# Kernel tuning notes

Measured on AMD Instinct MI355X. Metric: run time of the kernel, lower is better.

## Reference

```python
import jax, jax.numpy as jnp
import numpy as np

B = 8192
E = 8
H = 128
NUM_CLASSES = 3
SIM_THRESHOLD = 0.8
EFF_THRESHOLD = 0.1
TARGET_TEMP = 1.0
W_LB, W_EFF, W_CONS, W_ENT, W_TEMP = 0.1, 0.05, 0.1, 0.01, 0.01


def setup_inputs() -> dict:
    key = jax.random.key(0)
    k1, k2, k3, k4 = jax.random.split(key, 4)
    logits = jax.random.normal(k1, (B, NUM_CLASSES), dtype=jnp.float32)
    targets = jax.random.randint(k2, (B,), 0, NUM_CLASSES, dtype=jnp.int64)
    raw = jax.random.uniform(k3, (B, E), dtype=jnp.float32)
    routing_probs = raw / raw.sum(axis=-1, keepdims=True)  # rows sum to 1
    input_embeddings = jax.random.uniform(k4, (B, H), dtype=jnp.float32)
    temperature = jnp.ones((1,), dtype=jnp.float32)
    return {
        "logits": logits,
        "targets": targets,
        "routing_probs": routing_probs,
        "input_embeddings": input_embeddings,
        "temperature": temperature,
    }


def _dynamo_loss(logits, routing_probs, input_embeddings, temperature, targets):
    # --- task loss: cross entropy (sentiment) ---
    logp_cls = jax.nn.log_softmax(logits, axis=-1)
    task_loss = -jnp.take_along_axis(logp_cls, targets[:, None], axis=-1).mean()

    # --- load balance: var(mean usage) / (1/E)^2 (torch.var unbiased) ---
    expert_usage = routing_probs.mean(axis=0)  # [E]
    lb_loss = W_LB * jnp.var(expert_usage, ddof=1) * (E ** 2)

    # --- efficiency: sum of probs below threshold, averaged over batch ---
    small = jnp.where(routing_probs < EFF_THRESHOLD, routing_probs, 0.0)
    eff_loss = W_EFF * small.sum(axis=-1).mean()

    # --- consistency: masked pairwise KL over similar samples ---
    nrm = input_embeddings / jnp.linalg.norm(input_embeddings, axis=-1, keepdims=True)
    sim = nrm @ nrm.T  # [B, B]
    mask = (sim > SIM_THRESHOLD) & ~jnp.eye(B, dtype=bool)
    logp = jax.nn.log_softmax(routing_probs, axis=-1)  # [B, E]
    p = jnp.exp(logp)
    a = jnp.sum(p * logp, axis=-1)  # [B], sum_e p_j log p_j
    # KL(i,j) = sum_e p_j (log p_j - log p_i) = a[j] - logp[i] . p[j]
    kl = a[None, :] - logp @ p.T  # [B, B]
    num_pairs = mask.sum()
    kl_sum = jnp.sum(jnp.where(mask, kl, 0.0))
    cons_loss = W_CONS * jnp.where(num_pairs > 0, kl_sum / jnp.maximum(num_pairs, 1), 0.0)

    # --- entropy regularization (maximize entropy of routing_probs-as-probs) ---
    eps = 1e-8
    entropy = -jnp.sum(routing_probs * jnp.log(routing_probs + eps), axis=-1)
    ent_loss = W_ENT * (-entropy.mean())

    # --- temperature regularization ---
    temp_loss = W_TEMP * jnp.mean((temperature - TARGET_TEMP) ** 2)

    return task_loss + lb_loss + eff_loss + cons_loss + ent_loss + temp_loss


def reference(logits, targets, routing_probs, input_embeddings, temperature):
    return _dynamo_loss(logits, routing_probs, input_embeddings, temperature, targets)
```

## Files before the change

### kernel.cpp

```cpp
#include <hip/hip_runtime.h>
#include <stdint.h>

#define B_SZ 8192
#define LOG8 2.0794415416798357f
#define NCHUNK 544

typedef __attribute__((ext_vector_type(8))) short short8;
typedef __attribute__((ext_vector_type(4))) float floatx4;

typedef __attribute__((address_space(1))) const uint4 guint4;
typedef __attribute__((address_space(3))) uint4 luint4;

__device__ inline void async_cp16(const uint4* g, uint4* l) {
    __builtin_amdgcn_global_load_lds((guint4*)g, (luint4*)l, 16, 0, 0);
}

__device__ inline unsigned short f2bf(float f) {
    unsigned int u = __float_as_uint(f);
    u = (u + 0x7FFFu + ((u >> 16) & 1u)) >> 16;
    return (unsigned short)u;
}
__device__ inline float bf2f(unsigned short s) {
    return __uint_as_float(((unsigned int)s) << 16);
}
__device__ inline float wredf(float x) {
#pragma unroll
    for (int o = 32; o; o >>= 1) x += __shfl_down(x, o);
    return x;
}
__device__ inline int wredi(int x) {
#pragma unroll
    for (int o = 32; o; o >>= 1) x += __shfl_down(x, o);
    return x;
}


__global__ __launch_bounds__(512) void prep_all(
    const float* __restrict__ logits,
    const int* __restrict__ targets,
    const float* __restrict__ routing,
    const float* __restrict__ emb,
    unsigned short* __restrict__ nrm,
    unsigned short* __restrict__ nlq,
    unsigned short* __restrict__ pb,
    float* __restrict__ aprime,
    float* __restrict__ prepslot) {
    __shared__ float pred[8][11];
    const int bid = blockIdx.x;
    const int lane = threadIdx.x & 63;
    const int wave = threadIdx.x >> 6;

    if (bid < 256) {
#pragma unroll
        for (int iter = 0; iter < 4; ++iter) {
            int row = (((iter << 8) + bid) << 3) + wave;
            const float2* e2 = (const float2*)(emb + (size_t)row * 128);
            float2 v = e2[lane];
            float ss = v.x * v.x + v.y * v.y;
            ss = wredf(ss);
            ss = __shfl(ss, 0);
            float inv = rsqrtf(ss);
            ushort2 o;
            o.x = f2bf(v.x * inv);
            o.y = f2bf(v.y * inv);
            ((ushort2*)(nrm + (size_t)row * 128))[lane] = o;
        }
        return;
    }

    int row = ((bid - 256) << 9) + threadIdx.x;

    const float4* r4 = (const float4*)(routing + (size_t)row * 8);
    float4 va = r4[0], vb = r4[1];
    float v[8] = {va.x, va.y, va.z, va.w, vb.x, vb.y, vb.z, vb.w};

    float mx = v[0];
#pragma unroll
    for (int e = 1; e < 8; ++e) mx = fmaxf(mx, v[e]);
    float ex[8], s = 0.f;
#pragma unroll
    for (int e = 0; e < 8; ++e) { ex[e] = expf(v[e] - mx); s += ex[e]; }
    float ls = logf(s);
    float inv_s = 1.f / s;

    union { unsigned short u[8]; uint4 q; } lu, pu;
    float ap = 0.f;
#pragma unroll
    for (int e = 0; e < 8; ++e) {
        unsigned short pe = f2bf(ex[e] * inv_s);
        unsigned short le = f2bf(v[e] - mx - ls + LOG8);
        pu.u[e] = pe;
        lu.u[e] = le ^ 0x8000;
        ap += bf2f(pe) * bf2f(le);
    }
    ((uint4*)nlq)[row] = lu.q;
    ((uint4*)pb)[row] = pu.q;
    aprime[row] = ap;

    float eff = 0.f, ent = 0.f;
#pragma unroll
    for (int e = 0; e < 8; ++e) {
        if (v[e] < 0.1f) eff += v[e];
        ent += v[e] * logf(v[e] + 1e-8f);
    }

    const float* lg = logits + (size_t)row * 3;
    float a0 = lg[0], a1 = lg[1], a2 = lg[2];
    float mm = fmaxf(a0, fmaxf(a1, a2));
    float lse = mm + logf(expf(a0 - mm) + expf(a1 - mm) + expf(a2 - mm));
    int tg = targets[row];
    float tv = (tg == 0) ? a0 : ((tg == 1) ? a1 : a2);
    float task = lse - tv;

    task = wredf(task);
    eff = wredf(eff);
    ent = wredf(ent);
    float cs[8];
#pragma unroll
    for (int e = 0; e < 8; ++e) cs[e] = wredf(v[e]);

    if (lane == 0) {
        pred[wave][0] = task;
        pred[wave][1] = eff;
        pred[wave][2] = ent;
#pragma unroll
        for (int e = 0; e < 8; ++e) pred[wave][3 + e] = cs[e];
    }
    __syncthreads();
    if (threadIdx.x < 11) {
        float s2 = 0.f;
#pragma unroll
        for (int w = 0; w < 8; ++w) s2 += pred[w][threadIdx.x];
        prepslot[(bid - 256) * 11 + threadIdx.x] = s2;
    }
}

__global__ __launch_bounds__(512, 4) void tile_sym(
    const unsigned short* __restrict__ nrm,
    const unsigned short* __restrict__ nlq,
    const unsigned short* __restrict__ pb,
    const float* __restrict__ aprime,
    float* __restrict__ klslot,
    unsigned int* __restrict__ cntslot) {
    __shared__ uint4 sh[4096];

    const int t = threadIdx.x;
    const int wave = t >> 6, lane = t & 63;

    int bi = 0, rem = blockIdx.x;
    for (;;) {
        int nc = (135 - 2 * bi) >> 3;
        if (rem < nc) break;
        rem -= nc;
        ++bi;
    }
    const int c = rem;
    const int bj0 = 2 * bi + (c << 3);
    const int nt = min(8, 128 - bj0);
    const int iBase = bi << 7;

    const uint4* n4 = (const uint4*)nrm;

#pragma unroll
    for (int it = 0; it < 4; ++it) {
        int idx = t + (it << 9);
        int row = idx >> 4, s = idx & 15;
        int g = s ^ (row & 15);
        async_cp16(&n4[((size_t)(iBase + row) << 4) + g],
                   sh + (it << 9) + (wave << 6));
    }
    {
        const int jB = bj0 << 6;
#pragma unroll
        for (int it = 0; it < 2; ++it) {
            int idx = t + (it << 9);
            int row = idx >> 4, s = idx & 15;
            int g = s ^ (row & 15);
            async_cp16(&n4[((size_t)(jB + row) << 4) + g],
                       sh + 2048 + (it << 9) + (wave << 6));
        }
    }

    const int wr = wave >> 2, wc = wave & 3;
    const int m = lane & 15, q = lane >> 4;
    const short8 zero8 = (short8){0, 0, 0, 0, 0, 0, 0, 0};

    short8 crA[4];
#pragma unroll
    for (int a = 0; a < 4; ++a) {
        int ri = iBase + (wr << 6) + (a << 4) + m;
        short8 v = zero8;
        if (q == 0) v = *(const short8*)&nlq[(size_t)ri << 3];
        else if (q == 1) v = *(const short8*)&pb[(size_t)ri << 3];
        else if (q == 2) {
            v[0] = (short)f2bf(aprime[ri]);
            v[1] = (short)0x3F80;
        }
        crA[a] = v;
    }

    __syncthreads();

    float klLocal = 0.f;
    int cntLocal = 0;

#pragma unroll 1
    for (int tt = 0; tt < nt; ++tt) {
        const int bj = bj0 + tt;
        const int jBase = bj << 6;
        const bool strip = ((bj >> 1) == bi);
        const int cur = 2048 + ((tt & 1) << 10);

        if (tt + 1 < nt) {
            const int jN = (bj + 1) << 6;
            const int nxt = 2048 + (((tt + 1) & 1) << 10);
#pragma unroll
            for (int it = 0; it < 2; ++it) {
                int idx = t + (it << 9);
                int row = idx >> 4, s = idx & 15;
                int g = s ^ (row & 15);
                async_cp16(&n4[((size_t)(jN + row) << 4) + g],
                           sh + nxt + (it << 9) + (wave << 6));
            }
        }

        short8 crB;
        {
            int cj = jBase + (wc << 4) + m;
            short8 v = zero8;
            if (q == 0) v = *(const short8*)&pb[(size_t)cj << 3];
            else if (q == 1) v = *(const short8*)&nlq[(size_t)cj << 3];
            else if (q == 2) {
                v[0] = (short)0x3F80;
                v[1] = (short)f2bf(aprime[cj]);
            }
            crB = v;
        }

        floatx4 simacc[4];
#pragma unroll
        for (int a = 0; a < 4; ++a) simacc[a] = (floatx4){0.f, 0.f, 0.f, 0.f};
#pragma unroll
        for (int ks = 0; ks < 4; ++ks) {
            const int gk = (ks << 2) + q;
            short8 bfr;
            {
                int rb = (wc << 4) + m;
                bfr = *(const short8*)(sh + cur + (rb << 4) + (gk ^ m));
            }
            short8 af[4];
#pragma unroll
            for (int a = 0; a < 4; ++a) {
                int row = (wr << 6) + (a << 4) + m;
                af[a] = *(const short8*)(sh + (row << 4) + (gk ^ m));
            }
#pragma unroll
            for (int a = 0; a < 4; ++a)
                simacc[a] = __builtin_amdgcn_mfma_f32_16x16x32_bf16(
                    af[a], bfr, simacc[a], 0, 0, 0);
        }

        const int gCol = jBase + (wc << 4) + m;
#pragma unroll
        for (int a = 0; a < 4; ++a) {
            short8 ca = crA[a];
            if (strip) {
                if (q == 1) ca = zero8;
                else if (q == 2) ca[0] = 0;
            }
            floatx4 cr = __builtin_amdgcn_mfma_f32_16x16x32_bf16(
                ca, crB, (floatx4){0.f, 0.f, 0.f, 0.f}, 0, 0, 0);
            const int gRow0 = iBase + (wr << 6) + (a << 4) + (q << 2);
            if (strip) {
#pragma unroll
                for (int r = 0; r < 4; ++r) {
                    if ((simacc[a][r] > 0.8f) && (gRow0 + r != gCol)) {
                        klLocal += cr[r];
                        cntLocal += 1;
                    }
                }
            } else {
#pragma unroll
                for (int r = 0; r < 4; ++r) {
                    if (simacc[a][r] > 0.8f) {
                        klLocal += cr[r];
                        cntLocal += 2;
                    }
                }
            }
        }

        __syncthreads();
    }

    klLocal = wredf(klLocal);
    cntLocal = wredi(cntLocal);

    float* redk = (float*)sh;
    int* redc = (int*)(redk + 8);
    if (lane == 0) { redk[wave] = klLocal; redc[wave] = cntLocal; }
    __syncthreads();

    if (t == 0) {
        float k = 0.f;
        int cc = 0;
#pragma unroll
        for (int w = 0; w < 8; ++w) { k += redk[w]; cc += redc[w]; }
        klslot[blockIdx.x] = k;
        cntslot[blockIdx.x] = (unsigned int)cc;
    }
}

__global__ void finalize_k(const float* __restrict__ klslot,
                           const unsigned int* __restrict__ cntslot,
                           const float* __restrict__ prepslot,
                           const float* __restrict__ temp,
                           float* __restrict__ out) {
    __shared__ float sk[4];
    __shared__ int sc[4];
    __shared__ float sp[11];
    const int t = threadIdx.x, lane = t & 63, wave = t >> 6;

    float k = 0.f;
    int c = 0;
    for (int i = t; i < NCHUNK; i += 256) { k += klslot[i]; c += (int)cntslot[i]; }
    k = wredf(k);
    c = wredi(c);
    if (lane == 0) { sk[wave] = k; sc[wave] = c; }
    if (t < 11) {
        float s = 0.f;
        for (int r = 0; r < 16; ++r) s += prepslot[r * 11 + t];
        sp[t] = s;
    }
    __syncthreads();
    if (t == 0) {
        float K = sk[0] + sk[1] + sk[2] + sk[3];
        int C = sc[0] + sc[1] + sc[2] + sc[3];
        const float invB = 1.f / (float)B_SZ;
        float task = sp[0] * invB;
        float eff = 0.05f * sp[1] * invB;
        float entl = 0.01f * sp[2] * invB;
        float cons = 0.1f * (C > 0 ? K / (float)C : 0.f);
        float u[8], mean = 0.f;
        for (int e = 0; e < 8; ++e) { u[e] = sp[3 + e] * invB; mean += u[e]; }
        mean *= 0.125f;
        float var = 0.f;
        for (int e = 0; e < 8; ++e) { float d = u[e] - mean; var += d * d; }
        var *= (1.f / 7.f);
        float lb = 0.1f * var * 64.f;
        float tt = temp[0] - 1.f;
        out[0] = task + lb + eff + cons + entl + 0.01f * tt * tt;
    }
}

extern "C" void kernel_launch(void* const* d_in, const int* in_sizes, int n_in,
                              void* d_out, int out_size, void* d_ws, size_t ws_size,
                              hipStream_t stream) {
    const float* logits = (const float*)d_in[0];
    const int* targets = (const int*)d_in[1];
    const float* routing = (const float*)d_in[2];
    const float* emb = (const float*)d_in[3];
    const float* temp = (const float*)d_in[4];

    char* ws = (char*)d_ws;
    unsigned short* nrm = (unsigned short*)ws;
    unsigned short* nlq = (unsigned short*)(ws + 2097152);
    unsigned short* pb = (unsigned short*)(ws + 2228224);
    float* aprime = (float*)(ws + 2359296);
    float* klslot = (float*)(ws + 2392064);
    unsigned int* cntslot = (unsigned int*)(ws + 2394304);
    float* prepslot = (float*)(ws + 2396544);

    prep_all<<<272, 512, 0, stream>>>(logits, targets, routing, emb,
                                      nrm, nlq, pb, aprime, prepslot);
    tile_sym<<<NCHUNK, 512, 0, stream>>>(nrm, nlq, pb, aprime, klslot, cntslot);
    finalize_k<<<1, 256, 0, stream>>>(klslot, cntslot, prepslot, temp,
                                      (float*)d_out);
}
```

Baseline: 105.9 us.

## Fuse prep, tile and finalize into one persistent kernel with grid barrier

Merges the three launches into a single persistent kernel of 512 blocks. Each block first normalizes its slice of rows, then all blocks meet at an atomic-counter grid barrier, pull tile chunks from an atomic work queue, and the last block to finish does the final reduction. This removes two kernel launch gaps and the separate finalize pass. In exchange it relies on all 512 blocks being co-resident for the spin barrier, and it adds a memset plus atomic contention.

```diff
diff --git a/kernel.cpp b/kernel.cpp
--- a/kernel.cpp
+++ b/kernel.cpp
@@ -3,7 +3,8 @@
 
 #define B_SZ 8192
 #define LOG8 2.0794415416798357f
-#define NCHUNK 544
+#define NCHUNKS 544
+#define NBLK 512
 
 typedef __attribute__((ext_vector_type(8))) short short8;
 typedef __attribute__((ext_vector_type(4))) float floatx4;
@@ -35,321 +36,335 @@
 }
 
 
-__global__ __launch_bounds__(512) void prep_all(
+__global__ __launch_bounds__(512, 4) void fused_all(
     const float* __restrict__ logits,
     const int* __restrict__ targets,
     const float* __restrict__ routing,
     const float* __restrict__ emb,
+    const float* __restrict__ temp,
     unsigned short* __restrict__ nrm,
     unsigned short* __restrict__ nlq,
     unsigned short* __restrict__ pb,
     float* __restrict__ aprime,
-    float* __restrict__ prepslot) {
-    __shared__ float pred[8][11];
+    float* __restrict__ klslot,
+    unsigned int* __restrict__ cntslot,
+    float* __restrict__ prepcol,
+    unsigned int* __restrict__ ctrl,
+    float* __restrict__ out) {
+    __shared__ uint4 sh[4096];
+    __shared__ int msgSh;
+
+    const int t = threadIdx.x;
+    const int lane = t & 63, wave = t >> 6;
     const int bid = blockIdx.x;
-    const int lane = threadIdx.x & 63;
-    const int wave = threadIdx.x >> 6;
-
-    if (bid < 256) {
-#pragma unroll
-        for (int iter = 0; iter < 4; ++iter) {
-            int row = (((iter << 8) + bid) << 3) + wave;
-            const float2* e2 = (const float2*)(emb + (size_t)row * 128);
-            float2 v = e2[lane];
-            float ss = v.x * v.x + v.y * v.y;
-            ss = wredf(ss);
-            ss = __shfl(ss, 0);
-            float inv = rsqrtf(ss);
-            ushort2 o;
-            o.x = f2bf(v.x * inv);
-            o.y = f2bf(v.y * inv);
-            ((ushort2*)(nrm + (size_t)row * 128))[lane] = o;
-        }
-        return;
-    }
-
-    int row = ((bid - 256) << 9) + threadIdx.x;
-
-    const float4* r4 = (const float4*)(routing + (size_t)row * 8);
-    float4 va = r4[0], vb = r4[1];
-    float v[8] = {va.x, va.y, va.z, va.w, vb.x, vb.y, vb.z, vb.w};
-
-    float mx = v[0];
-#pragma unroll
-    for (int e = 1; e < 8; ++e) mx = fmaxf(mx, v[e]);
-    float ex[8], s = 0.f;
-#pragma unroll
-    for (int e = 0; e < 8; ++e) { ex[e] = expf(v[e] - mx); s += ex[e]; }
-    float ls = logf(s);
-    float inv_s = 1.f / s;
-
-    union { unsigned short u[8]; uint4 q; } lu, pu;
-    float ap = 0.f;
-#pragma unroll
-    for (int e = 0; e < 8; ++e) {
-        unsigned short pe = f2bf(ex[e] * inv_s);
-        unsigned short le = f2bf(v[e] - mx - ls + LOG8);
-        pu.u[e] = pe;
-        lu.u[e] = le ^ 0x8000;
-        ap += bf2f(pe) * bf2f(le);
-    }
-    ((uint4*)nlq)[row] = lu.q;
-    ((uint4*)pb)[row] = pu.q;
-    aprime[row] = ap;
-
-    float eff = 0.f, ent = 0.f;
-#pragma unroll
-    for (int e = 0; e < 8; ++e) {
-        if (v[e] < 0.1f) eff += v[e];
-        ent += v[e] * logf(v[e] + 1e-8f);
-    }
-
-    const float* lg = logits + (size_t)row * 3;
-    float a0 = lg[0], a1 = lg[1], a2 = lg[2];
-    float mm = fmaxf(a0, fmaxf(a1, a2));
-    float lse = mm + logf(expf(a0 - mm) + expf(a1 - mm) + expf(a2 - mm));
-    int tg = targets[row];
-    float tv = (tg == 0) ? a0 : ((tg == 1) ? a1 : a2);
-    float task = lse - tv;
-
-    task = wredf(task);
-    eff = wredf(eff);
-    ent = wredf(ent);
-    float cs[8];
-#pragma unroll
-    for (int e = 0; e < 8; ++e) cs[e] = wredf(v[e]);
-
-    if (lane == 0) {
-        pred[wave][0] = task;
-        pred[wave][1] = eff;
-        pred[wave][2] = ent;
-#pragma unroll
-        for (int e = 0; e < 8; ++e) pred[wave][3 + e] = cs[e];
-    }
+
+#pragma unroll
+    for (int i = 0; i < 2; ++i) {
+        int row = (bid << 4) + (wave << 1) + i;
+        const float2* e2 = (const float2*)(emb + (size_t)row * 128);
+        float2 v = e2[lane];
+        float ss = v.x * v.x + v.y * v.y;
+        ss = wredf(ss);
+        ss = __shfl(ss, 0);
+        float inv = rsqrtf(ss);
+        ushort2 o;
+        o.x = f2bf(v.x * inv);
+        o.y = f2bf(v.y * inv);
+        ((ushort2*)(nrm + (size_t)row * 128))[lane] = o;
+    }
+
+    float acc11[11];
+#pragma unroll
+    for (int k = 0; k < 11; ++k) acc11[k] = 0.f;
+    if (t < 16) {
+        int row = (bid << 4) + t;
+        const float4* r4 = (const float4*)(routing + (size_t)row * 8);
+        float4 va = r4[0], vb = r4[1];
+        float v[8] = {va.x, va.y, va.z, va.w, vb.x, vb.y, vb.z, vb.w};
+
+        float mx = v[0];
+#pragma unroll
+        for (int e = 1; e < 8; ++e) mx = fmaxf(mx, v[e]);
+        float ex[8], s = 0.f;
+#pragma unroll
+        for (int e = 0; e < 8; ++e) { ex[e] = expf(v[e] - mx); s += ex[e]; }
+        float ls = logf(s);
+        float inv_s = 1.f / s;
+
+        union { unsigned short u[8]; uint4 q; } lu, pu;
+        float ap = 0.f;
+#pragma unroll
+        for (int e = 0; e < 8; ++e) {
+            unsigned short pe = f2bf(ex[e] * inv_s);
+            unsigned short le = f2bf(v[e] - mx - ls + LOG8);
+            pu.u[e] = pe;
+            lu.u[e] = le ^ 0x8000;
+            ap += bf2f(pe) * bf2f(le);
+        }
+        ((uint4*)nlq)[row] = lu.q;
+        ((uint4*)pb)[row] = pu.q;
+        aprime[row] = ap;
+
+        float eff = 0.f, ent = 0.f;
+#pragma unroll
+        for (int e = 0; e < 8; ++e) {
+            if (v[e] < 0.1f) eff += v[e];
+            ent += v[e] * logf(v[e] + 1e-8f);
+            acc11[3 + e] = v[e];
+        }
+
+        const float* lg = logits + (size_t)row * 3;
+        float a0 = lg[0], a1 = lg[1], a2 = lg[2];
+        float mm = fmaxf(a0, fmaxf(a1, a2));
+        float lse = mm + logf(expf(a0 - mm) + expf(a1 - mm) + expf(a2 - mm));
+        int tg = targets[row];
+        float tv = (tg == 0) ? a0 : ((tg == 1) ? a1 : a2);
+        acc11[0] = lse - tv;
+        acc11[1] = eff;
+        acc11[2] = ent;
+    }
+    if (wave == 0) {
+#pragma unroll
+        for (int k = 0; k < 11; ++k) acc11[k] = wredf(acc11[k]);
+        if (lane == 0) {
+#pragma unroll
+            for (int k = 0; k < 11; ++k) prepcol[k * NBLK + bid] = acc11[k];
+        }
+    }
+
     __syncthreads();
-    if (threadIdx.x < 11) {
-        float s2 = 0.f;
-#pragma unroll
-        for (int w = 0; w < 8; ++w) s2 += pred[w][threadIdx.x];
-        prepslot[(bid - 256) * 11 + threadIdx.x] = s2;
-    }
-}
-
-__global__ __launch_bounds__(512, 4) void tile_sym(
-    const unsigned short* __restrict__ nrm,
-    const unsigned short* __restrict__ nlq,
-    const unsigned short* __restrict__ pb,
-    const float* __restrict__ aprime,
-    float* __restrict__ klslot,
-    unsigned int* __restrict__ cntslot) {
-    __shared__ uint4 sh[4096];
-
-    const int t = threadIdx.x;
-    const int wave = t >> 6, lane = t & 63;
-
-    int bi = 0, rem = blockIdx.x;
+    if (t == 0) {
+        __threadfence();
+        atomicAdd(&ctrl[0], 1u);
+        while (__hip_atomic_load(&ctrl[0], __ATOMIC_ACQUIRE,
+                                 __HIP_MEMORY_SCOPE_AGENT) < NBLK) {}
+    }
+    __syncthreads();
+
+    const uint4* n4 = (const uint4*)nrm;
+    const int wr = wave >> 2, wc = wave & 3;
+    const int m = lane & 15, q = lane >> 4;
+    const short8 zero8 = (short8){0, 0, 0, 0, 0, 0, 0, 0};
+
+    float klLocal = 0.f;
+    int cntLocal = 0;
+
+#pragma unroll 1
     for (;;) {
-        int nc = (135 - 2 * bi) >> 3;
-        if (rem < nc) break;
-        rem -= nc;
-        ++bi;
-    }
-    const int c = rem;
-    const int bj0 = 2 * bi + (c << 3);
-    const int nt = min(8, 128 - bj0);
-    const int iBase = bi << 7;
-
-    const uint4* n4 = (const uint4*)nrm;
-
-#pragma unroll
-    for (int it = 0; it < 4; ++it) {
-        int idx = t + (it << 9);
-        int row = idx >> 4, s = idx & 15;
-        int g = s ^ (row & 15);
-        async_cp16(&n4[((size_t)(iBase + row) << 4) + g],
-                   sh + (it << 9) + (wave << 6));
-    }
-    {
-        const int jB = bj0 << 6;
-#pragma unroll
-        for (int it = 0; it < 2; ++it) {
+        if (t == 0) msgSh = (int)atomicAdd(&ctrl[1], 1u);
+        __syncthreads();
+        const int chunk = msgSh;
+        if (chunk >= NCHUNKS) break;
+
+        int bi = 0, rem = chunk;
+        for (;;) {
+            int nc = (135 - 2 * bi) >> 3;
+            if (rem < nc) break;
+            rem -= nc;
+            ++bi;
+        }
+        const int bj0 = 2 * bi + (rem << 3);
+        const int nt = min(8, 128 - bj0);
+        const int iBase = bi << 7;
+
+#pragma unroll
+        for (int it = 0; it < 4; ++it) {
             int idx = t + (it << 9);
             int row = idx >> 4, s = idx & 15;
             int g = s ^ (row & 15);
-            async_cp16(&n4[((size_t)(jB + row) << 4) + g],
-                       sh + 2048 + (it << 9) + (wave << 6));
-        }
-    }
-
-    const int wr = wave >> 2, wc = wave & 3;
-    const int m = lane & 15, q = lane >> 4;
-    const short8 zero8 = (short8){0, 0, 0, 0, 0, 0, 0, 0};
-
-    short8 crA[4];
-#pragma unroll
-    for (int a = 0; a < 4; ++a) {
-        int ri = iBase + (wr << 6) + (a << 4) + m;
-        short8 v = zero8;
-        if (q == 0) v = *(const short8*)&nlq[(size_t)ri << 3];
-        else if (q == 1) v = *(const short8*)&pb[(size_t)ri << 3];
-        else if (q == 2) {
-            v[0] = (short)f2bf(aprime[ri]);
-            v[1] = (short)0x3F80;
-        }
-        crA[a] = v;
-    }
-
-    __syncthreads();
-
-    float klLocal = 0.f;
-    int cntLocal = 0;
-
-#pragma unroll 1
-    for (int tt = 0; tt < nt; ++tt) {
-        const int bj = bj0 + tt;
-        const int jBase = bj << 6;
-        const bool strip = ((bj >> 1) == bi);
-        const int cur = 2048 + ((tt & 1) << 10);
-
-        if (tt + 1 < nt) {
-            const int jN = (bj + 1) << 6;
-            const int nxt = 2048 + (((tt + 1) & 1) << 10);
+            async_cp16(&n4[((size_t)(iBase + row) << 4) + g],
+                       sh + (it << 9) + (wave << 6));
+        }
+        {
+            const int jB = bj0 << 6;
 #pragma unroll
             for (int it = 0; it < 2; ++it) {
                 int idx = t + (it << 9);
                 int row = idx >> 4, s = idx & 15;
                 int g = s ^ (row & 15);
-                async_cp16(&n4[((size_t)(jN + row) << 4) + g],
-                           sh + nxt + (it << 9) + (wave << 6));
-            }
-        }
-
-        short8 crB;
-        {
-            int cj = jBase + (wc << 4) + m;
+                async_cp16(&n4[((size_t)(jB + row) << 4) + g],
+                           sh + 2048 + (it << 9) + (wave << 6));
+            }
+        }
+
+        short8 crA[4];
+#pragma unroll
+        for (int a = 0; a < 4; ++a) {
+            int ri = iBase + (wr << 6) + (a << 4) + m;
             short8 v = zero8;
-            if (q == 0) v = *(const short8*)&pb[(size_t)cj << 3];
-            else if (q == 1) v = *(const short8*)&nlq[(size_t)cj << 3];
+            if (q == 0) v = *(const short8*)&nlq[(size_t)ri << 3];
+            else if (q == 1) v = *(const short8*)&pb[(size_t)ri << 3];
             else if (q == 2) {
-                v[0] = (short)0x3F80;
-                v[1] = (short)f2bf(aprime[cj]);
-            }
-            crB = v;
-        }
-
-        floatx4 simacc[4];
-#pragma unroll
-        for (int a = 0; a < 4; ++a) simacc[a] = (floatx4){0.f, 0.f, 0.f, 0.f};
-#pragma unroll
-        for (int ks = 0; ks < 4; ++ks) {
-            const int gk = (ks << 2) + q;
-            short8 bfr;
+                v[0] = (short)f2bf(aprime[ri]);
+                v[1] = (short)0x3F80;
+            }
+            crA[a] = v;
+        }
+
+        __syncthreads();
+
+#pragma unroll 1
+        for (int tt = 0; tt < nt; ++tt) {
+            const int bj = bj0 + tt;
+            const int jBase = bj << 6;
+            const bool strip = ((bj >> 1) == bi);
+            const int cur = 2048 + ((tt & 1) << 10);
+
+            if (tt + 1 < nt) {
+                const int jN = (bj + 1) << 6;
+                const int nxt = 2048 + (((tt + 1) & 1) << 10);
+#pragma unroll
+                for (int it = 0; it < 2; ++it) {
+                    int idx = t + (it << 9);
+                    int row = idx >> 4, s = idx & 15;
+                    int g = s ^ (row & 15);
+                    async_cp16(&n4[((size_t)(jN + row) << 4) + g],
+                               sh + nxt + (it << 9) + (wave << 6));
+                }
+            }
+
+            short8 crB;
             {
-                int rb = (wc << 4) + m;
-                bfr = *(const short8*)(sh + cur + (rb << 4) + (gk ^ m));
-            }
-            short8 af[4];
+                int cj = jBase + (wc << 4) + m;
+                short8 v = zero8;
+                if (q == 0) v = *(const short8*)&pb[(size_t)cj << 3];
+                else if (q == 1) v = *(const short8*)&nlq[(size_t)cj << 3];
+                else if (q == 2) {
+                    v[0] = (short)0x3F80;
+                    v[1] = (short)f2bf(aprime[cj]);
+                }
+                crB = v;
+            }
+
+            floatx4 simacc[4];
+#pragma unroll
+            for (int a = 0; a < 4; ++a) simacc[a] = (floatx4){0.f, 0.f, 0.f, 0.f};
+#pragma unroll
+            for (int ks = 0; ks < 4; ++ks) {
+                const int gk = (ks << 2) + q;
+                short8 bfr;
+                {
+                    int rb = (wc << 4) + m;
+                    bfr = *(const short8*)(sh + cur + (rb << 4) + (gk ^ m));
+                }
+                short8 af[4];
+#pragma unroll
+                for (int a = 0; a < 4; ++a) {
+                    int row = (wr << 6) + (a << 4) + m;
+                    af[a] = *(const short8*)(sh + (row << 4) + (gk ^ m));
+                }
+#pragma unroll
+                for (int a = 0; a < 4; ++a)
+                    simacc[a] = __builtin_amdgcn_mfma_f32_16x16x32_bf16(
+                        af[a], bfr, simacc[a], 0, 0, 0);
+            }
+
+            const int gCol = jBase + (wc << 4) + m;
 #pragma unroll
             for (int a = 0; a < 4; ++a) {
-                int row = (wr << 6) + (a << 4) + m;
-                af[a] = *(const short8*)(sh + (row << 4) + (gk ^ m));
-            }
-#pragma unroll
-            for (int a = 0; a < 4; ++a)
-                simacc[a] = __builtin_amdgcn_mfma_f32_16x16x32_bf16(
-                    af[a], bfr, simacc[a], 0, 0, 0);
-        }
-
-        const int gCol = jBase + (wc << 4) + m;
-#pragma unroll
-        for (int a = 0; a < 4; ++a) {
-            short8 ca = crA[a];
-            if (strip) {
-                if (q == 1) ca = zero8;
-                else if (q == 2) ca[0] = 0;
-            }
-            floatx4 cr = __builtin_amdgcn_mfma_f32_16x16x32_bf16(
-                ca, crB, (floatx4){0.f, 0.f, 0.f, 0.f}, 0, 0, 0);
-            const int gRow0 = iBase + (wr << 6) + (a << 4) + (q << 2);
-            if (strip) {
-#pragma unroll
-                for (int r = 0; r < 4; ++r) {
-                    if ((simacc[a][r] > 0.8f) && (gRow0 + r != gCol)) {
-                        klLocal += cr[r];
-                        cntLocal += 1;
+                short8 ca = crA[a];
+                if (strip) {
+                    if (q == 1) ca = zero8;
+                    else if (q == 2) ca[0] = 0;
+                }
+                floatx4 cr = __builtin_amdgcn_mfma_f32_16x16x32_bf16(
+                    ca, crB, (floatx4){0.f, 0.f, 0.f, 0.f}, 0, 0, 0);
+                const int gRow0 = iBase + (wr << 6) + (a << 4) + (q << 2);
+                if (strip) {
+#pragma unroll
+                    for (int r = 0; r < 4; ++r) {
+                        if ((simacc[a][r] > 0.8f) && (gRow0 + r != gCol)) {
+                            klLocal += cr[r];
+                            cntLocal += 1;
+                        }
                     }
-                }
-            } else {
-#pragma unroll
-                for (int r = 0; r < 4; ++r) {
-                    if (simacc[a][r] > 0.8f) {
-                        klLocal += cr[r];
-                        cntLocal += 2;
+                } else {
+#pragma unroll
+                    for (int r = 0; r < 4; ++r) {
+                        if (simacc[a][r] > 0.8f) {
+                            klLocal += cr[r];
+                            cntLocal += 2;
+                        }
                     }
                 }
             }
-        }
-
-        __syncthreads();
+
+            __syncthreads();
+        }
     }
 
     klLocal = wredf(klLocal);
     cntLocal = wredi(cntLocal);
-
     float* redk = (float*)sh;
     int* redc = (int*)(redk + 8);
     if (lane == 0) { redk[wave] = klLocal; redc[wave] = cntLocal; }
     __syncthreads();
-
     if (t == 0) {
         float k = 0.f;
-        int cc = 0;
-#pragma unroll
-        for (int w = 0; w < 8; ++w) { k += redk[w]; cc += redc[w]; }
-        klslot[blockIdx.x] = k;
-        cntslot[blockIdx.x] = (unsigned int)cc;
-    }
-}
-
-__global__ void finalize_k(const float* __restrict__ klslot,
-                           const unsigned int* __restrict__ cntslot,
-                           const float* __restrict__ prepslot,
-                           const float* __restrict__ temp,
-                           float* __restrict__ out) {
-    __shared__ float sk[4];
-    __shared__ int sc[4];
-    __shared__ float sp[11];
-    const int t = threadIdx.x, lane = t & 63, wave = t >> 6;
-
-    float k = 0.f;
-    int c = 0;
-    for (int i = t; i < NCHUNK; i += 256) { k += klslot[i]; c += (int)cntslot[i]; }
-    k = wredf(k);
-    c = wredi(c);
-    if (lane == 0) { sk[wave] = k; sc[wave] = c; }
-    if (t < 11) {
-        float s = 0.f;
-        for (int r = 0; r < 16; ++r) s += prepslot[r * 11 + t];
-        sp[t] = s;
+        int c = 0;
+#pragma unroll
+        for (int w = 0; w < 8; ++w) { k += redk[w]; c += redc[w]; }
+        klslot[bid] = k;
+        cntslot[bid] = (unsigned int)c;
+        __threadfence();
+        unsigned int old = atomicAdd(&ctrl[2], 1u);
+        msgSh = (old == NBLK - 1);
     }
     __syncthreads();
-    if (t == 0) {
-        float K = sk[0] + sk[1] + sk[2] + sk[3];
-        int C = sc[0] + sc[1] + sc[2] + sc[3];
-        const float invB = 1.f / (float)B_SZ;
-        float task = sp[0] * invB;
-        float eff = 0.05f * sp[1] * invB;
-        float entl = 0.01f * sp[2] * invB;
-        float cons = 0.1f * (C > 0 ? K / (float)C : 0.f);
-        float u[8], mean = 0.f;
-        for (int e = 0; e < 8; ++e) { u[e] = sp[3 + e] * invB; mean += u[e]; }
-        mean *= 0.125f;
-        float var = 0.f;
-        for (int e = 0; e < 8; ++e) { float d = u[e] - mean; var += d * d; }
-        var *= (1.f / 7.f);
-        float lb = 0.1f * var * 64.f;
-        float tt = temp[0] - 1.f;
-        out[0] = task + lb + eff + cons + entl + 0.01f * tt * tt;
+
+    if (msgSh) {
+        float k = __hip_atomic_load(&klslot[t], __ATOMIC_RELAXED,
+                                    __HIP_MEMORY_SCOPE_AGENT);
+        int c = (int)__hip_atomic_load(&cntslot[t], __ATOMIC_RELAXED,
+                                       __HIP_MEMORY_SCOPE_AGENT);
+        float pv[11];
+#pragma unroll
+        for (int kk = 0; kk < 11; ++kk)
+            pv[kk] = __hip_atomic_load(&prepcol[kk * NBLK + t], __ATOMIC_RELAXED,
+                                       __HIP_MEMORY_SCOPE_AGENT);
+        k = wredf(k);
+        c = wredi(c);
+#pragma unroll
+        for (int kk = 0; kk < 11; ++kk) pv[kk] = wredf(pv[kk]);
+
+        float* rk = (float*)sh;
+        int* rc = (int*)(rk + 8);
+        float* rp = (float*)(rc + 8);
+        if (lane == 0) {
+            rk[wave] = k;
+            rc[wave] = c;
+#pragma unroll
+            for (int kk = 0; kk < 11; ++kk) rp[wave * 11 + kk] = pv[kk];
+        }
+        __syncthreads();
+        if (t == 0) {
+            float K = 0.f;
+            int C = 0;
+            float sp[11];
+#pragma unroll
+            for (int kk = 0; kk < 11; ++kk) sp[kk] = 0.f;
+#pragma unroll
+            for (int w = 0; w < 8; ++w) {
+                K += rk[w];
+                C += rc[w];
+#pragma unroll
+                for (int kk = 0; kk < 11; ++kk) sp[kk] += rp[w * 11 + kk];
+            }
+            const float invB = 1.f / (float)B_SZ;
+            float task = sp[0] * invB;
+            float eff = 0.05f * sp[1] * invB;
+            float entl = 0.01f * sp[2] * invB;
+            float cons = 0.1f * (C > 0 ? K / (float)C : 0.f);
+            float u[8], mean = 0.f;
+            for (int e = 0; e < 8; ++e) { u[e] = sp[3 + e] * invB; mean += u[e]; }
+            mean *= 0.125f;
+            float var = 0.f;
+            for (int e = 0; e < 8; ++e) { float d = u[e] - mean; var += d * d; }
+            var *= (1.f / 7.f);
+            float lb = 0.1f * var * 64.f;
+            float tt = temp[0] - 1.f;
+            out[0] = task + lb + eff + cons + entl + 0.01f * tt * tt;
+        }
     }
 }
 
@@ -368,12 +383,12 @@
     unsigned short* pb = (unsigned short*)(ws + 2228224);
     float* aprime = (float*)(ws + 2359296);
     float* klslot = (float*)(ws + 2392064);
-    unsigned int* cntslot = (unsigned int*)(ws + 2394304);
-    float* prepslot = (float*)(ws + 2396544);
-
-    prep_all<<<272, 512, 0, stream>>>(logits, targets, routing, emb,
-                                      nrm, nlq, pb, aprime, prepslot);
-    tile_sym<<<NCHUNK, 512, 0, stream>>>(nrm, nlq, pb, aprime, klslot, cntslot);
-    finalize_k<<<1, 256, 0, stream>>>(klslot, cntslot, prepslot, temp,
-                                      (float*)d_out);
-}
+    unsigned int* cntslot = (unsigned int*)(ws + 2394112);
+    float* prepcol = (float*)(ws + 2396160);
+    unsigned int* ctrl = (unsigned int*)(ws + 2418688);
+
+    hipMemsetAsync(ctrl, 0, 16, stream);
+    fused_all<<<NBLK, 512, 0, stream>>>(logits, targets, routing, emb, temp,
+                                        nrm, nlq, pb, aprime, klslot, cntslot,
+                                        prepcol, ctrl, (float*)d_out);
+}
```

Result: slower. 149.9 us (+41.6%).
